# Kernel optimization log

Measured on AMD Instinct MI355X. Metric: run time of the kernel, lower is better.

## Reference

```python
import jax, jax.numpy as jnp
import numpy as np

DT_MIN, DT_MAX = 1e-3, 0.1
BSZ, SEQ, DM, DS = 8, 2048, 1024, 16


def setup_inputs() -> dict:
    key = jax.random.key(0)
    ks = jax.random.split(key, 8)
    x = jax.random.normal(ks[0], (BSZ, SEQ, DM), jnp.float32)
    a_log = jax.random.normal(ks[1], (DM, DS), jnp.float32) * -0.5
    b = jax.random.normal(ks[2], (DM, DS), jnp.float32) * 0.02
    c = jax.random.normal(ks[3], (DM, DS), jnp.float32) * 0.02
    dt_w = jax.random.normal(ks[4], (DM, DM), jnp.float32) * (1.0 / np.sqrt(DM))
    dt_b = jnp.zeros((DM,), jnp.float32)
    conv_w = jax.random.normal(ks[5], (DM, 1, 3), jnp.float32) * (1.0 / np.sqrt(3.0))
    conv_b = jnp.zeros((DM,), jnp.float32)
    return {"x": x, "a_log": a_log, "b": b, "c": c, "dt_w": dt_w, "dt_b": dt_b, "conv_w": conv_w, "conv_b": conv_b}


def _depthwise_conv(x, conv_w, conv_b):
    # x: (B,N,C) -> (B,C,N) depthwise conv k=3, pad=1 -> (B,N,C)
    xc = jnp.transpose(x, (0, 2, 1))
    y = jax.lax.conv_general_dilated(
        xc, conv_w, window_strides=(1,), padding=[(1, 1)],
        feature_group_count=xc.shape[1],
        dimension_numbers=("NCH", "OIH", "NCH"))
    y = y + conv_b[None, :, None]
    return jnp.transpose(y, (0, 2, 1))


def reference(x, a_log, b, c, dt_w, dt_b, conv_w, conv_b):
    Bn, N, C = x.shape
    D = a_log.shape[1]
    xf = _depthwise_conv(x, conv_w, conv_b)                      # (B,N,C)
    dt = jax.nn.sigmoid(xf @ dt_w.T + dt_b) * (DT_MAX - DT_MIN) + DT_MIN  # (B,N,C)
    A = -jax.nn.softplus(a_log)                                   # (C,D)

    def step(s, inp):
        xt, dtt = inp                                             # each (B,C)
        expA = jnp.exp(dtt[..., None] * A)                        # (B,C,D)
        s = expA * s + (dtt * xt)[..., None] * b                  # (B,C,D)
        y = jnp.einsum("bcd,cd->bc", s, c)
        return s, y

    s0 = jnp.zeros((Bn, C, D), x.dtype)
    xs = (jnp.transpose(xf, (1, 0, 2)), jnp.transpose(dt, (1, 0, 2)))
    _, ys = jax.lax.scan(step, s0, xs)                            # (N,B,C)
    return jnp.transpose(ys, (1, 0, 2))                           # (B,N,C)
```

## Files before the change

kernel.cpp:

```cpp
#include <hip/hip_runtime.h>
#include <stdint.h>

#define BSZ 8
#define SEQ 2048
#define DM 1024
#define DS 16
#define MROWS (BSZ * SEQ)
#define CHK 64
#define CLEN (SEQ / CHK)
#define LOG2E 1.4426950408889634f

typedef __bf16 bf16x8 __attribute__((ext_vector_type(8)));
typedef float f32x4 __attribute__((ext_vector_type(4)));

union F4 { float4 v; float f[4]; };

__device__ __forceinline__ uint16_t f2bf(float f) {
  uint32_t u = __float_as_uint(f);
  u += 0x7FFFu + ((u >> 16) & 1u);
  return (uint16_t)(u >> 16);
}

__device__ __forceinline__ uint32_t pack_h2(float a, float b) {
  _Float16 ha = (_Float16)a, hb = (_Float16)b;
  uint16_t ua = __builtin_bit_cast(uint16_t, ha);
  uint16_t ub = __builtin_bit_cast(uint16_t, hb);
  return (uint32_t)ua | ((uint32_t)ub << 16);
}
__device__ __forceinline__ float unpack_lo(uint32_t v) {
  return (float)__builtin_bit_cast(_Float16, (uint16_t)(v & 0xffffu));
}
__device__ __forceinline__ float unpack_hi(uint32_t v) {
  return (float)__builtin_bit_cast(_Float16, (uint16_t)(v >> 16));
}

__device__ __forceinline__ void async_cp16(const void* g, void* l) {
  __builtin_amdgcn_global_load_lds(
      (const __attribute__((address_space(1))) uint32_t*)(uintptr_t)g,
      (__attribute__((address_space(3))) uint32_t*)(uint32_t)(uintptr_t)l,
      16, 0, 0);
}

__global__ __launch_bounds__(256) void wprep_kernel(
    const float* __restrict__ w, uint16_t* __restrict__ wb) {
  int t = blockIdx.x * 256 + threadIdx.x;
  F4 u; u.v = *(const float4*)(w + (size_t)t * 4);
  uint32_t lo = f2bf(u.f[0]) | ((uint32_t)f2bf(u.f[1]) << 16);
  uint32_t hi = f2bf(u.f[2]) | ((uint32_t)f2bf(u.f[3]) << 16);
  *(uint2*)(wb + (size_t)t * 4) = make_uint2(lo, hi);
}

__global__ __launch_bounds__(256) void aprep_kernel(
    const float* __restrict__ a_log, const float* __restrict__ bm,
    const float* __restrict__ cm, float* __restrict__ A2c,
    float* __restrict__ A2t, float* __restrict__ cb2) {
  int e = blockIdx.x * 256 + threadIdx.x;
  float a = a_log[e];
  float A2 = -log1pf(__expf(a)) * LOG2E;
  A2c[e] = A2;
  cb2[e] = bm[e] * cm[e];
  int c = e >> 4, d = e & 15;
  int j = d >> 2, i = d & 3;
  A2t[((size_t)j * DM + c) * 4 + i] = A2;
}

__global__ __launch_bounds__(256) void conv_kernel(
    const float* __restrict__ x, const float* __restrict__ cw,
    const float* __restrict__ cb, uint16_t* __restrict__ xf) {
  int t = blockIdx.x * 256 + threadIdx.x;
  int cg = t & (DM / 4 - 1);
  int bn = t >> 8;
  int n = bn & (SEQ - 1);
  int c0 = cg * 4;
  const float* row = x + (size_t)bn * DM + c0;
  F4 xm, xc, xp;
  xm.v = make_float4(0.f, 0.f, 0.f, 0.f);
  xp.v = make_float4(0.f, 0.f, 0.f, 0.f);
  xc.v = *(const float4*)row;
  if (n > 0)       xm.v = *(const float4*)(row - DM);
  if (n < SEQ - 1) xp.v = *(const float4*)(row + DM);
  uint16_t o[4];
#pragma unroll
  for (int j = 0; j < 4; ++j) {
    int c = c0 + j;
    float v = cw[c * 3 + 0] * xm.f[j] + cw[c * 3 + 1] * xc.f[j] +
              cw[c * 3 + 2] * xp.f[j] + cb[c];
    o[j] = f2bf(v);
  }
  uint32_t lo = o[0] | ((uint32_t)o[1] << 16);
  uint32_t hi = o[2] | ((uint32_t)o[3] << 16);
  *(uint2*)(xf + (size_t)bn * DM + c0) = make_uint2(lo, hi);
}

__global__ __launch_bounds__(256) void gemm_kernel(
    const uint16_t* __restrict__ A,
    const uint16_t* __restrict__ B,
    const float* __restrict__ bias,
    uint32_t* __restrict__ ud) {
  __shared__ __align__(16) uint16_t As[128 * 64];
  __shared__ __align__(16) uint16_t Bs[128 * 64];
  const int tid = threadIdx.x;
  const int w = tid >> 6;
  const int L = tid & 63;
  const int wm = w & 1, wn = w >> 1;
  const int lane15 = L & 15, q = L >> 4;
  const int m0 = blockIdx.y * 128;
  const int n0 = blockIdx.x * 128;
  const int lr = L >> 3;
  const int lc = (((L & 7) ^ lr)) * 8;
  const int r7 = lane15 & 7;

  f32x4 acc[4][4] = {};

  for (int kt = 0; kt < DM; kt += 64) {
#pragma unroll
    for (int r = 0; r < 4; ++r) {
      int R = (r * 4 + w) * 8;
      async_cp16(A + (size_t)(m0 + R + lr) * DM + kt + lc, &As[R * 64]);
    }
#pragma unroll
    for (int r = 0; r < 4; ++r) {
      int R = (r * 4 + w) * 8;
      async_cp16(B + (size_t)(n0 + R + lr) * DM + kt + lc, &Bs[R * 64]);
    }
    __syncthreads();
#pragma unroll
    for (int ks = 0; ks < 64; ks += 32) {
      bf16x8 af[4], bfr[4];
      const int jbase = ks >> 3;
#pragma unroll
      for (int mi = 0; mi < 4; ++mi)
        af[mi] = *(const bf16x8*)(As + (wm * 64 + mi * 16 + lane15) * 64 +
                                  (((jbase + q) ^ r7) << 3));
#pragma unroll
      for (int ni = 0; ni < 4; ++ni)
        bfr[ni] = *(const bf16x8*)(Bs + (wn * 64 + ni * 16 + lane15) * 64 +
                                   (((jbase + q) ^ r7) << 3));
#pragma unroll
      for (int mi = 0; mi < 4; ++mi)
#pragma unroll
        for (int ni = 0; ni < 4; ++ni)
          acc[mi][ni] = __builtin_amdgcn_mfma_f32_16x16x32_bf16(
              af[mi], bfr[ni], acc[mi][ni], 0, 0, 0);
    }
    __syncthreads();
  }

#pragma unroll
  for (int ni = 0; ni < 4; ++ni) {
    int col = n0 + wn * 64 + ni * 16 + lane15;
    float db = bias[col];
#pragma unroll
    for (int mi = 0; mi < 4; ++mi) {
      int rowb = m0 + wm * 64 + mi * 16 + q * 4;
#pragma unroll
      for (int r = 0; r < 4; ++r) {
        size_t idx = (size_t)(rowb + r) * DM + col;
        float z = acc[mi][ni][r] + db;
        float dtv = 0.099f / (1.f + __expf(-z)) + 0.001f;
        float xfv = __uint_as_float((uint32_t)A[idx] << 16);
        ud[idx] = pack_h2(dtv * xfv, dtv);
      }
    }
  }
}


__global__ __launch_bounds__(256) void scan_part1(
    const uint32_t* __restrict__ ud, const float* __restrict__ A2c,
    float* __restrict__ F, float* __restrict__ Sdt) {
  const int c = blockIdx.x * 256 + threadIdx.x;
  const int k = blockIdx.y;
  const int b = blockIdx.z;
  const int n0 = k * CLEN;

  float A2[DS], s[DS];
#pragma unroll
  for (int j = 0; j < 4; ++j) {
    F4 ua; ua.v = *(const float4*)(A2c + (size_t)c * DS + j * 4);
#pragma unroll
    for (int i = 0; i < 4; ++i) {
      A2[j * 4 + i] = ua.f[i];
      s[j * 4 + i] = 0.f;
    }
  }

  const uint32_t* up = ud + ((size_t)b * SEQ + n0) * DM + c;
  uint32_t c0 = up[0];
  uint32_t c1 = up[DM];
  float sdt = 0.f;

  for (int t = 0; t < CLEN; ++t) {
    uint32_t c2 = 0;
    if (t + 2 < CLEN) c2 = up[(size_t)(t + 2) * DM];
    float uv = unpack_lo(c0);
    float dtv = unpack_hi(c0);
    sdt += dtv;
#pragma unroll
    for (int d = 0; d < DS; ++d) {
      float e = __builtin_amdgcn_exp2f(dtv * A2[d]);
      s[d] = fmaf(e, s[d], uv);
    }
    c0 = c1; c1 = c2;
  }

  const size_t kk = (size_t)b * CHK + k;
#pragma unroll
  for (int j = 0; j < 4; ++j) {
    F4 fo;
#pragma unroll
    for (int i = 0; i < 4; ++i) fo.f[i] = s[j * 4 + i];
    *(float4*)(F + ((kk * 4 + j) * DM + c) * 4) = fo.v;
  }
  Sdt[kk * DM + c] = sdt;
}

__global__ __launch_bounds__(256) void scan_combine(
    float* __restrict__ F, const float* __restrict__ Sdt,
    const float* __restrict__ A2t) {
  const int t = blockIdx.x * 256 + threadIdx.x;
  const int b = blockIdx.y;
  const int c = (t >> 2) & (DM - 1);
  const float A2 = A2t[t];
  const size_t stride = (size_t)DM * DS;
  const size_t base = (size_t)b * CHK * stride + t;
  const size_t sbase = (size_t)b * CHK * DM + c;
  float carry = 0.f;
#pragma unroll 4
  for (int k = 0; k < CHK; ++k) {
    const size_t idx = base + (size_t)k * stride;
    float f = F[idx];
    float p = __builtin_amdgcn_exp2f(A2 * Sdt[sbase + (size_t)k * DM]);
    F[idx] = carry;
    carry = fmaf(p, carry, f);
  }
}

__global__ __launch_bounds__(256) void scan_part3(
    const uint32_t* __restrict__ ud, const float* __restrict__ A2c,
    const float* __restrict__ cb2m, const float* __restrict__ Sin,
    float* __restrict__ out) {
  const int c = blockIdx.x * 256 + threadIdx.x;
  const int k = blockIdx.y;
  const int b = blockIdx.z;
  const int n0 = k * CLEN;

  float A2[DS], cb2[DS], s[DS];
  const size_t kk = (size_t)b * CHK + k;
#pragma unroll
  for (int j = 0; j < 4; ++j) {
    F4 ua, uc, us;
    ua.v = *(const float4*)(A2c + (size_t)c * DS + j * 4);
    uc.v = *(const float4*)(cb2m + (size_t)c * DS + j * 4);
    us.v = *(const float4*)(Sin + ((kk * 4 + j) * DM + c) * 4);
#pragma unroll
    for (int i = 0; i < 4; ++i) {
      A2[j * 4 + i] = ua.f[i];
      cb2[j * 4 + i] = uc.f[i];
      s[j * 4 + i] = us.f[i];
    }
  }

  const uint32_t* up = ud + ((size_t)b * SEQ + n0) * DM + c;
  float* op = out + ((size_t)b * SEQ + n0) * DM + c;
  uint32_t c0 = up[0];
  uint32_t c1 = up[DM];

  for (int t = 0; t < CLEN; ++t) {
    uint32_t c2 = 0;
    if (t + 2 < CLEN) c2 = up[(size_t)(t + 2) * DM];
    float uv = unpack_lo(c0);
    float dtv = unpack_hi(c0);
    float y0 = 0.f, y1 = 0.f;
#pragma unroll
    for (int d = 0; d < DS; d += 2) {
      float e0 = __builtin_amdgcn_exp2f(dtv * A2[d]);
      float e1 = __builtin_amdgcn_exp2f(dtv * A2[d + 1]);
      s[d] = fmaf(e0, s[d], uv);
      s[d + 1] = fmaf(e1, s[d + 1], uv);
      y0 = fmaf(cb2[d], s[d], y0);
      y1 = fmaf(cb2[d + 1], s[d + 1], y1);
    }
    op[(size_t)t * DM] = y0 + y1;
    c0 = c1; c1 = c2;
  }
}

extern "C" void kernel_launch(void* const* d_in, const int* in_sizes, int n_in,
                              void* d_out, int out_size, void* d_ws, size_t ws_size,
                              hipStream_t stream) {
  const float* x     = (const float*)d_in[0];
  const float* a_log = (const float*)d_in[1];
  const float* bm    = (const float*)d_in[2];
  const float* cm    = (const float*)d_in[3];
  const float* dt_w  = (const float*)d_in[4];
  const float* dt_b  = (const float*)d_in[5];
  const float* cw    = (const float*)d_in[6];
  const float* cb    = (const float*)d_in[7];
  float* out = (float*)d_out;

  char* ws = (char*)d_ws;
  uint16_t* xf_bf = (uint16_t*)ws;
  uint16_t* w_bf  = (uint16_t*)(ws + (size_t)MROWS * DM * 2);
  uint32_t* ud = (uint32_t*)(ws + (size_t)MROWS * DM * 2 + (size_t)DM * DM * 2);
  float* Fbuf = (float*)(ud + (size_t)MROWS * DM);
  float* Sdt  = Fbuf + (size_t)BSZ * CHK * DM * DS;
  float* A2c  = Sdt + (size_t)BSZ * CHK * DM;
  float* A2t  = A2c + (size_t)DM * DS;
  float* cb2  = A2t + (size_t)DM * DS;

  hipLaunchKernelGGL(wprep_kernel, dim3(DM * DM / 1024), dim3(256), 0, stream,
                     dt_w, w_bf);
  hipLaunchKernelGGL(aprep_kernel, dim3(DM * DS / 256), dim3(256), 0, stream,
                     a_log, bm, cm, A2c, A2t, cb2);
  hipLaunchKernelGGL(conv_kernel, dim3(MROWS * DM / 1024), dim3(256), 0, stream,
                     x, cw, cb, xf_bf);
  hipLaunchKernelGGL(gemm_kernel, dim3(DM / 128, MROWS / 128), dim3(256), 0,
                     stream, xf_bf, w_bf, dt_b, ud);
  hipLaunchKernelGGL(scan_part1, dim3(DM / 256, CHK, BSZ), dim3(256), 0, stream,
                     ud, A2c, Fbuf, Sdt);
  hipLaunchKernelGGL(scan_combine, dim3(DM * DS / 256, BSZ), dim3(256), 0,
                     stream, Fbuf, Sdt, A2t);
  hipLaunchKernelGGL(scan_part3, dim3(DM / 256, CHK, BSZ), dim3(256), 0, stream,
                     ud, A2c, cb2, Fbuf, out);
}
```

Baseline: 297.4 us.

## Reuse GEMM LDS tile for xf epilogue, deepen scan prefetch, split combine output

The GEMM epilogue now takes the xf values it needs from the A tile already in LDS, during the k-iteration that lines up with the output columns, and keeps them in registers instead of reloading xf from global memory. The scan part1 and part3 loops prefetch three steps ahead and unroll by four. scan_combine software-prefetches the next chunk's F and Sdt values and writes carries to a separate buffer that reuses the dead xf_bf region. The cost is 32 extra registers per thread in the GEMM, which may lower occupancy.

```diff
diff --git a/kernel.cpp b/kernel.cpp
--- a/kernel.cpp
+++ b/kernel.cpp
@@ -111,6 +111,8 @@
   const int r7 = lane15 & 7;
 
   f32x4 acc[4][4] = {};
+  uint32_t xst[4][4][2];
+  const int ktmatch = n0 + wn * 64;
 
   for (int kt = 0; kt < DM; kt += 64) {
 #pragma unroll
@@ -124,6 +126,23 @@
       async_cp16(B + (size_t)(n0 + R + lr) * DM + kt + lc, &Bs[R * 64]);
     }
     __syncthreads();
+
+    if (kt == ktmatch) {
+#pragma unroll
+      for (int mi = 0; mi < 4; ++mi)
+#pragma unroll
+        for (int ni = 0; ni < 4; ++ni)
+#pragma unroll
+          for (int rp = 0; rp < 2; ++rp) {
+            int row0 = wm * 64 + mi * 16 + q * 4 + rp * 2;
+            int row1 = row0 + 1;
+            int cc = ni * 16 + lane15;
+            uint32_t e0 = As[row0 * 64 + (((cc >> 3) ^ (row0 & 7)) << 3) + (cc & 7)];
+            uint32_t e1 = As[row1 * 64 + (((cc >> 3) ^ (row1 & 7)) << 3) + (cc & 7)];
+            xst[mi][ni][rp] = e0 | (e1 << 16);
+          }
+    }
+
 #pragma unroll
     for (int ks = 0; ks < 64; ks += 32) {
       bf16x8 af[4], bfr[4];
@@ -158,7 +177,9 @@
         size_t idx = (size_t)(rowb + r) * DM + col;
         float z = acc[mi][ni][r] + db;
         float dtv = 0.099f / (1.f + __expf(-z)) + 0.001f;
-        float xfv = __uint_as_float((uint32_t)A[idx] << 16);
+        uint32_t p = xst[mi][ni][r >> 1];
+        uint32_t bits = (r & 1) ? (p & 0xffff0000u) : (p << 16);
+        float xfv = __uint_as_float(bits);
         ud[idx] = pack_h2(dtv * xfv, dtv);
       }
     }
@@ -188,11 +209,13 @@
   const uint32_t* up = ud + ((size_t)b * SEQ + n0) * DM + c;
   uint32_t c0 = up[0];
   uint32_t c1 = up[DM];
+  uint32_t c2 = up[2 * DM];
   float sdt = 0.f;
 
+#pragma unroll 4
   for (int t = 0; t < CLEN; ++t) {
-    uint32_t c2 = 0;
-    if (t + 2 < CLEN) c2 = up[(size_t)(t + 2) * DM];
+    int tn = (t + 3 < CLEN) ? t + 3 : CLEN - 1;
+    uint32_t c3 = up[(size_t)tn * DM];
     float uv = unpack_lo(c0);
     float dtv = unpack_hi(c0);
     sdt += dtv;
@@ -201,7 +224,7 @@
       float e = __builtin_amdgcn_exp2f(dtv * A2[d]);
       s[d] = fmaf(e, s[d], uv);
     }
-    c0 = c1; c1 = c2;
+    c0 = c1; c1 = c2; c2 = c3;
   }
 
   const size_t kk = (size_t)b * CHK + k;
@@ -216,8 +239,8 @@
 }
 
 __global__ __launch_bounds__(256) void scan_combine(
-    float* __restrict__ F, const float* __restrict__ Sdt,
-    const float* __restrict__ A2t) {
+    const float* __restrict__ F, float* __restrict__ Sin,
+    const float* __restrict__ Sdt, const float* __restrict__ A2t) {
   const int t = blockIdx.x * 256 + threadIdx.x;
   const int b = blockIdx.y;
   const int c = (t >> 2) & (DM - 1);
@@ -226,13 +249,17 @@
   const size_t base = (size_t)b * CHK * stride + t;
   const size_t sbase = (size_t)b * CHK * DM + c;
   float carry = 0.f;
+  float fcur = F[base];
+  float scur = Sdt[sbase];
 #pragma unroll 4
   for (int k = 0; k < CHK; ++k) {
-    const size_t idx = base + (size_t)k * stride;
-    float f = F[idx];
-    float p = __builtin_amdgcn_exp2f(A2 * Sdt[sbase + (size_t)k * DM]);
-    F[idx] = carry;
-    carry = fmaf(p, carry, f);
+    int kn = (k + 1 < CHK) ? k + 1 : CHK - 1;
+    float fnext = F[base + (size_t)kn * stride];
+    float snext = Sdt[sbase + (size_t)kn * DM];
+    float p = __builtin_amdgcn_exp2f(A2 * scur);
+    Sin[base + (size_t)k * stride] = carry;
+    carry = fmaf(p, carry, fcur);
+    fcur = fnext; scur = snext;
   }
 }
 
@@ -265,10 +292,12 @@
   float* op = out + ((size_t)b * SEQ + n0) * DM + c;
   uint32_t c0 = up[0];
   uint32_t c1 = up[DM];
-
+  uint32_t c2 = up[2 * DM];
+
+#pragma unroll 4
   for (int t = 0; t < CLEN; ++t) {
-    uint32_t c2 = 0;
-    if (t + 2 < CLEN) c2 = up[(size_t)(t + 2) * DM];
+    int tn = (t + 3 < CLEN) ? t + 3 : CLEN - 1;
+    uint32_t c3 = up[(size_t)tn * DM];
     float uv = unpack_lo(c0);
     float dtv = unpack_hi(c0);
     float y0 = 0.f, y1 = 0.f;
@@ -282,7 +311,7 @@
       y1 = fmaf(cb2[d + 1], s[d + 1], y1);
     }
     op[(size_t)t * DM] = y0 + y1;
-    c0 = c1; c1 = c2;
+    c0 = c1; c1 = c2; c2 = c3;
   }
 }
 
@@ -302,6 +331,7 @@
   char* ws = (char*)d_ws;
   uint16_t* xf_bf = (uint16_t*)ws;
   uint16_t* w_bf  = (uint16_t*)(ws + (size_t)MROWS * DM * 2);
+  float*    Sin   = (float*)ws;
   uint32_t* ud = (uint32_t*)(ws + (size_t)MROWS * DM * 2 + (size_t)DM * DM * 2);
   float* Fbuf = (float*)(ud + (size_t)MROWS * DM);
   float* Sdt  = Fbuf + (size_t)BSZ * CHK * DM * DS;
@@ -320,7 +350,7 @@
   hipLaunchKernelGGL(scan_part1, dim3(DM / 256, CHK, BSZ), dim3(256), 0, stream,
                      ud, A2c, Fbuf, Sdt);
   hipLaunchKernelGGL(scan_combine, dim3(DM * DS / 256, BSZ), dim3(256), 0,
-                     stream, Fbuf, Sdt, A2t);
+                     stream, Fbuf, Sin, Sdt, A2t);
   hipLaunchKernelGGL(scan_part3, dim3(DM / 256, CHK, BSZ), dim3(256), 0, stream,
-                     ud, A2c, cb2, Fbuf, out);
-}
+                     ud, A2c, cb2, Sin, out);
+}
```

Result: faster. 289.0 us (-2.8%).
